# Optimization experiments

Measured on AMD Instinct MI355X. Metric: run time of the kernel, lower is better.

Reference implementation:

```python
import jax, jax.numpy as jnp
import numpy as np

B, S, D = 2, 2048, 768
E, L = 4, 2
H = 4 * D  # dim_mlp = dim * mlp_ratio
EPS = 1e-6


def setup_inputs() -> dict:
    key = jax.random.key(0)
    ks = jax.random.split(key, 4)
    x = jax.random.normal(ks[0], (B, S, D), dtype=jnp.float32)
    expert_idx = jax.random.randint(ks[1], (B, S), 0, E, dtype=jnp.int32)
    # Linear weights: normal(std=0.02), biases zero (per init_weights).
    W1 = 0.02 * jax.random.normal(ks[2], (L, E, D, H), dtype=jnp.float32)
    b1 = jnp.zeros((L, E, H), dtype=jnp.float32)
    W2 = 0.02 * jax.random.normal(ks[3], (L, E, H, D), dtype=jnp.float32)
    b2 = jnp.zeros((L, E, D), dtype=jnp.float32)
    # LayerNorm: weight=1, bias=0 (per init_weights).
    ln_g = jnp.ones((L, D), dtype=jnp.float32)
    ln_b = jnp.zeros((L, D), dtype=jnp.float32)
    return {"x": x, "expert_idx": expert_idx, "W1": W1, "b1": b1,
            "W2": W2, "b2": b2, "ln_g": ln_g, "ln_b": ln_b}


def _layernorm(x, g, b):
    mu = jnp.mean(x, axis=-1, keepdims=True)
    var = jnp.mean(jnp.square(x - mu), axis=-1, keepdims=True)
    return (x - mu) * jax.lax.rsqrt(var + EPS) * g + b


def reference(x, expert_idx, W1, b1, W2, b2, ln_g, ln_b):
    # Eval mode: Dropout and DropPath are identity.
    idx = expert_idx[:, :, None, None]  # [B,S,1,1] for gather over expert axis
    for i in range(L):
        h = _layernorm(x, ln_g[i], ln_b[i])                       # [B,S,D]
        # All experts' FFNs computed densely (as in the torch module).
        a = jnp.einsum('bsd,edh->bseh', h, W1[i]) + b1[i]         # [B,S,E,H]
        a = jax.nn.gelu(a, approximate=False)                     # exact GELU (nn.GELU)
        y = jnp.einsum('bseh,ehd->bsed', a, W2[i]) + b2[i]        # [B,S,E,D] == feat_all
        # Per-token gather of the selected expert's slice.
        sel = jnp.take_along_axis(y, idx, axis=2)[:, :, 0, :]     # [B,S,D]
        x = x + sel
    return x
```

## Files before the change

### kernel.cpp

```cpp
#include <hip/hip_runtime.h>
#include <hip/hip_bf16.h>

#define T_TOK 4096
#define DD 768
#define HH 3072
#define EE 4
#define LL 2

typedef __attribute__((ext_vector_type(8))) short short8;
typedef __attribute__((ext_vector_type(4))) float f32x4;

__device__ __forceinline__ float bf2f(ushort u) { return __uint_as_float(((unsigned)u) << 16); }
__device__ __forceinline__ ushort f2bf(float f) {
  unsigned x = __float_as_uint(f);
  return (ushort)((x + 0x7fffu + ((x >> 16) & 1u)) >> 16);
}

__device__ __forceinline__ void gl2lds16(const void* g, void* l) {
  __builtin_amdgcn_global_load_lds((const __attribute__((address_space(1))) void*)g,
                                   (__attribute__((address_space(3))) void*)l, 16, 0, 0);
}

__global__ __launch_bounds__(256) void prep_kernel(const int* __restrict__ eidx,
                                                   int* __restrict__ perm,
                                                   int* __restrict__ inv,
                                                   int* __restrict__ meta) {
  __shared__ int cnt[EE], cur[EE], offs[EE];
  int t = threadIdx.x;
  if (t < EE) { cnt[t] = 0; cur[t] = 0; }
  __syncthreads();
  for (int i = t; i < T_TOK; i += 256) atomicAdd(&cnt[eidx[i]], 1);
  __syncthreads();
  if (t == 0) {
    int off = 0, nt = 0;
    for (int e = 0; e < EE; e++) {
      meta[e] = off; offs[e] = off;
      int c = cnt[e];
      int n = (c + 127) >> 7;
      for (int k = 0; k < n; k++) { meta[6 + nt] = e; meta[46 + nt] = k << 7; nt++; }
      off += c;
    }
    meta[4] = off;
    meta[5] = nt;
  }
  __syncthreads();
  for (int i = t; i < T_TOK; i += 256) {
    int e = eidx[i];
    int pos = offs[e] + atomicAdd(&cur[e], 1);
    perm[pos] = i;
    inv[i] = pos;
  }
}

__global__ __launch_bounds__(256) void cvt_kernel(const float* __restrict__ x,
                                                  float* __restrict__ xf, int n) {
  int i = blockIdx.x * 256 + threadIdx.x;
  int stride = gridDim.x * 256;
  for (; i < n; i += stride) xf[i] = x[i];
}

__global__ __launch_bounds__(256) void store_kernel(const float* __restrict__ xf,
                                                    float* __restrict__ out, int n) {
  int i = blockIdx.x * 256 + threadIdx.x;
  int stride = gridDim.x * 256;
  for (; i < n; i += stride) out[i] = xf[i];
}

__global__ __launch_bounds__(256) void ln_kernel(const float* __restrict__ xf,
                                                 const float* __restrict__ g,
                                                 const float* __restrict__ b,
                                                 const int* __restrict__ inv,
                                                 ushort* __restrict__ h) {
  int wid = blockIdx.x * 4 + (threadIdx.x >> 6);
  int lane = threadIdx.x & 63;
  const float* xr = xf + (size_t)wid * DD;
  float v[12], s = 0.f, ss = 0.f;
#pragma unroll
  for (int i = 0; i < 12; i++) {
    v[i] = xr[lane + i * 64];
    s += v[i]; ss += v[i] * v[i];
  }
#pragma unroll
  for (int o = 32; o; o >>= 1) { s += __shfl_xor(s, o, 64); ss += __shfl_xor(ss, o, 64); }
  float mu = s * (1.f / DD);
  float var = ss * (1.f / DD) - mu * mu;
  float rs = rsqrtf(var + 1e-6f);
  ushort* hr = h + (size_t)inv[wid] * DD;
#pragma unroll
  for (int i = 0; i < 12; i++) {
    int c = lane + i * 64;
    hr[c] = f2bf((v[i] - mu) * rs * g[c] + b[c]);
  }
}

__global__ __launch_bounds__(256) void transpose_f32_bf16(const float* __restrict__ src,
                                                          ushort* __restrict__ dst,
                                                          int R, int C) {
  __shared__ ushort tile[64][68];
  size_t mo = (size_t)blockIdx.z * R * C;
  src += mo;
  dst += mo;
  int c0 = blockIdx.x * 64, r0 = blockIdx.y * 64;
  int t = threadIdx.x;
  int tr = t >> 4;
  int tc = (t & 15) << 2;
#pragma unroll
  for (int i = 0; i < 4; i++) {
    int r = tr + i * 16;
    float4 v = *(const float4*)(src + (size_t)(r0 + r) * C + (c0 + tc));
    tile[r][tc] = f2bf(v.x); tile[r][tc + 1] = f2bf(v.y);
    tile[r][tc + 2] = f2bf(v.z); tile[r][tc + 3] = f2bf(v.w);
  }
  __syncthreads();
#pragma unroll
  for (int i = 0; i < 4; i++) {
    int c = tr + i * 16;
    ushort4 v;
    v.x = tile[tc][c]; v.y = tile[tc + 1][c]; v.z = tile[tc + 2][c]; v.w = tile[tc + 3][c];
    *(ushort4*)(dst + (size_t)(c0 + c) * R + (r0 + tc)) = v;
  }
}

template <int KTOT, int KLEN, int NTOT, bool GELU>
__global__ __launch_bounds__(256) void gemm_kernel(const ushort* __restrict__ A,
                                                   const ushort* __restrict__ Bt,
                                                   const float* __restrict__ bias,
                                                   void* __restrict__ Cout,
                                                   const int* __restrict__ perm,
                                                   const int* __restrict__ meta) {
  int ty = blockIdx.y;
  if (ty >= meta[5]) return;
  int e = meta[6 + ty];
  int mstart = meta[46 + ty];
  int off0 = meta[e];
  int cnt = meta[e + 1] - off0;
  if (cnt <= 0) return;
  int ntile = blockIdx.x;
  int kbegin = blockIdx.z * KLEN;

  __shared__ __align__(16) ushort lds[16384];
  ushort* As = lds;
  ushort* Bs = lds + 8192;

  int tid = threadIdx.x;
  int w = tid >> 6, lane = tid & 63;

  int rr = lane >> 3;
  int koff = (lane & 7) * 8;
  const ushort* agp[4];
  const ushort* bgp[4];
  ushort* alp[4];
  ushort* blp[4];
#pragma unroll
  for (int i = 0; i < 4; i++) {
    int r = w * 32 + i * 8 + rr;
    int arow = off0 + min(mstart + r, cnt - 1);
    int brow = e * NTOT + ntile * 128 + r;
    agp[i] = A + (size_t)arow * KTOT + kbegin + koff;
    bgp[i] = Bt + (size_t)brow * KTOT + kbegin + koff;
    alp[i] = As + r * 64 + koff;
    blp[i] = Bs + r * 64 + koff;
  }

  int wm = (w >> 1) * 64, wn = (w & 1) * 64;
  int qm = lane & 15;
  int qk = (lane >> 4) * 8;

  f32x4 acc[4][4];
#pragma unroll
  for (int mi = 0; mi < 4; mi++)
#pragma unroll
    for (int ni = 0; ni < 4; ni++) acc[mi][ni] = (f32x4){0.f, 0.f, 0.f, 0.f};

  for (int k0 = 0; k0 < KLEN; k0 += 64) {
#pragma unroll
    for (int i = 0; i < 4; i++) {
      gl2lds16(agp[i] + k0, alp[i]);
      gl2lds16(bgp[i] + k0, blp[i]);
    }
    __syncthreads();
#pragma unroll
    for (int h2 = 0; h2 < 2; h2++) {
      short8 af[4], bfr[4];
#pragma unroll
      for (int mi = 0; mi < 4; mi++)
        af[mi] = *(const short8*)(As + (wm + mi * 16 + qm) * 64 + h2 * 32 + qk);
#pragma unroll
      for (int ni = 0; ni < 4; ni++)
        bfr[ni] = *(const short8*)(Bs + (wn + ni * 16 + qm) * 64 + h2 * 32 + qk);
#pragma unroll
      for (int mi = 0; mi < 4; mi++)
#pragma unroll
        for (int ni = 0; ni < 4; ni++)
          acc[mi][ni] = __builtin_amdgcn_mfma_f32_16x16x32_bf16(af[mi], bfr[ni], acc[mi][ni], 0, 0, 0);
    }
    __syncthreads();
  }

  int rbase = (lane >> 4) * 4;
  if (GELU) {
    float bv[4];
#pragma unroll
    for (int ni = 0; ni < 4; ni++)
      bv[ni] = bias[e * NTOT + ntile * 128 + wn + ni * 16 + qm];
#pragma unroll
    for (int mi = 0; mi < 4; mi++)
#pragma unroll
      for (int ni = 0; ni < 4; ni++) {
        int c = wn + ni * 16 + qm;
#pragma unroll
        for (int r = 0; r < 4; r++) {
          float vv = acc[mi][ni][r] + bv[ni];
          vv = 0.5f * vv * (1.f + erff(vv * 0.70710678118f));
          lds[(wm + mi * 16 + rbase + r) * 128 + c] = f2bf(vv);
        }
      }
    __syncthreads();
    int row0 = tid >> 4;
    int cseg = (tid & 15) * 8;
    ushort* aout = (ushort*)Cout;
#pragma unroll
    for (int it = 0; it < 8; it++) {
      int row = it * 16 + row0;
      int mg = mstart + row;
      if (mg < cnt) {
        short8 v = *(const short8*)(lds + row * 128 + cseg);
        *(short8*)(aout + (size_t)(off0 + mg) * HH + ntile * 128 + cseg) = v;
      }
    }
  } else {
    float* xf = (float*)Cout;
    float bv[4];
#pragma unroll
    for (int ni = 0; ni < 4; ni++)
      bv[ni] = (blockIdx.z == 0) ? bias[e * NTOT + ntile * 128 + wn + ni * 16 + qm] : 0.f;
#pragma unroll
    for (int mi = 0; mi < 4; mi++) {
#pragma unroll
      for (int r = 0; r < 4; r++) {
        int mg = mstart + wm + mi * 16 + rbase + r;
        if (mg >= cnt) continue;
        int token = perm[off0 + mg];
        float* crow = xf + (size_t)token * DD + ntile * 128;
#pragma unroll
        for (int ni = 0; ni < 4; ni++)
          atomicAdd(&crow[wn + ni * 16 + qm], acc[mi][ni][r] + bv[ni]);
      }
    }
  }
}

extern "C" void kernel_launch(void* const* d_in, const int* in_sizes, int n_in,
                              void* d_out, int out_size, void* d_ws, size_t ws_size,
                              hipStream_t stream) {
  const float* x   = (const float*)d_in[0];
  const int*   eidx = (const int*)d_in[1];
  const float* W1  = (const float*)d_in[2];
  const float* b1  = (const float*)d_in[3];
  const float* W2  = (const float*)d_in[4];
  const float* b2  = (const float*)d_in[5];
  const float* lng = (const float*)d_in[6];
  const float* lnb = (const float*)d_in[7];

  char* ws = (char*)d_ws;
  float*  xf   = (float*)(ws + 0);
  ushort* h    = (ushort*)(ws + 12582912);
  ushort* a    = (ushort*)(ws + 18874368);
  ushort* Wt   = (ushort*)(ws + 44040192);
  int*    perm = (int*)(ws + 62914560);
  int*    inv  = (int*)(ws + 62930944);
  int*    meta = (int*)(ws + 62947328);

  const int NELT = T_TOK * DD;

  prep_kernel<<<1, 256, 0, stream>>>(eidx, perm, inv, meta);
  cvt_kernel<<<3072, 256, 0, stream>>>(x, xf, NELT);

  for (int l = 0; l < LL; l++) {
    ln_kernel<<<T_TOK / 4, 256, 0, stream>>>(xf, lng + l * DD, lnb + l * DD, inv, h);
    transpose_f32_bf16<<<dim3(HH / 64, DD / 64, EE), 256, 0, stream>>>(
        W1 + (size_t)l * EE * DD * HH, Wt, DD, HH);
    gemm_kernel<DD, DD, HH, true><<<dim3(HH / 128, 36), 256, 0, stream>>>(
        h, Wt, b1 + l * EE * HH, (void*)a, perm, meta);
    transpose_f32_bf16<<<dim3(DD / 64, HH / 64, EE), 256, 0, stream>>>(
        W2 + (size_t)l * EE * HH * DD, Wt, HH, DD);
    gemm_kernel<HH, HH / 2, DD, false><<<dim3(DD / 128, 36, 2), 256, 0, stream>>>(
        a, Wt, b2 + l * EE * DD, (void*)xf, perm, meta);
  }

  store_kernel<<<3072, 256, 0, stream>>>(xf, (float*)d_out, NELT);
}
```

Measured before the change: 440.6 us.

## Replace atomic scatter with split-K partial buffers, smaller M tiles, swizzled LDS

The down-projection GEMM now writes its two split-K partials as plain stores into sorted-order buffers instead of atomically adding into the token-order residual. The residual sum is folded into the next layer's LayerNorm and into a final store kernel, and the copy-in kernel and perm array are removed. GEMM M tiles shrink from 128 to 64 rows with an XOR-swizzled LDS layout, which gives more blocks and fewer bank conflicts. The cost is extra partial-buffer traffic and lower per-block reuse of the B tiles.

```diff
diff --git a/kernel.cpp b/kernel.cpp
--- a/kernel.cpp
+++ b/kernel.cpp
@@ -6,6 +6,7 @@
 #define HH 3072
 #define EE 4
 #define LL 2
+#define NELT (T_TOK * DD)
 
 typedef __attribute__((ext_vector_type(8))) short short8;
 typedef __attribute__((ext_vector_type(4))) float f32x4;
@@ -22,7 +23,6 @@
 }
 
 __global__ __launch_bounds__(256) void prep_kernel(const int* __restrict__ eidx,
-                                                   int* __restrict__ perm,
                                                    int* __restrict__ inv,
                                                    int* __restrict__ meta) {
   __shared__ int cnt[EE], cur[EE], offs[EE];
@@ -36,8 +36,8 @@
     for (int e = 0; e < EE; e++) {
       meta[e] = off; offs[e] = off;
       int c = cnt[e];
-      int n = (c + 127) >> 7;
-      for (int k = 0; k < n; k++) { meta[6 + nt] = e; meta[46 + nt] = k << 7; nt++; }
+      int n = (c + 63) >> 6;
+      for (int k = 0; k < n; k++) { meta[8 + nt] = e; meta[96 + nt] = k << 6; nt++; }
       off += c;
     }
     meta[4] = off;
@@ -46,50 +46,62 @@
   __syncthreads();
   for (int i = t; i < T_TOK; i += 256) {
     int e = eidx[i];
-    int pos = offs[e] + atomicAdd(&cur[e], 1);
-    perm[pos] = i;
-    inv[i] = pos;
-  }
-}
-
-__global__ __launch_bounds__(256) void cvt_kernel(const float* __restrict__ x,
-                                                  float* __restrict__ xf, int n) {
-  int i = blockIdx.x * 256 + threadIdx.x;
-  int stride = gridDim.x * 256;
-  for (; i < n; i += stride) xf[i] = x[i];
-}
-
-__global__ __launch_bounds__(256) void store_kernel(const float* __restrict__ xf,
-                                                    float* __restrict__ out, int n) {
-  int i = blockIdx.x * 256 + threadIdx.x;
-  int stride = gridDim.x * 256;
-  for (; i < n; i += stride) out[i] = xf[i];
-}
-
-__global__ __launch_bounds__(256) void ln_kernel(const float* __restrict__ xf,
+    inv[i] = offs[e] + atomicAdd(&cur[e], 1);
+  }
+}
+
+template <bool HASY, bool WRITEX>
+__global__ __launch_bounds__(256) void ln_kernel(const float* __restrict__ x,
+                                                 const float* __restrict__ y,
                                                  const float* __restrict__ g,
                                                  const float* __restrict__ b,
                                                  const int* __restrict__ inv,
-                                                 ushort* __restrict__ h) {
+                                                 ushort* __restrict__ h,
+                                                 float* __restrict__ xf) {
   int wid = blockIdx.x * 4 + (threadIdx.x >> 6);
   int lane = threadIdx.x & 63;
-  const float* xr = xf + (size_t)wid * DD;
+  int pos = inv[wid];
+  const float* xr = x + (size_t)wid * DD;
+  const float* y0 = y + (size_t)pos * DD;
+  const float* y1 = y0 + NELT;
   float v[12], s = 0.f, ss = 0.f;
 #pragma unroll
   for (int i = 0; i < 12; i++) {
-    v[i] = xr[lane + i * 64];
-    s += v[i]; ss += v[i] * v[i];
+    int c = lane + i * 64;
+    float vv = xr[c];
+    if (HASY) vv += y0[c] + y1[c];
+    if (WRITEX) xf[(size_t)wid * DD + c] = vv;
+    v[i] = vv;
+    s += vv; ss += vv * vv;
   }
 #pragma unroll
   for (int o = 32; o; o >>= 1) { s += __shfl_xor(s, o, 64); ss += __shfl_xor(ss, o, 64); }
   float mu = s * (1.f / DD);
   float var = ss * (1.f / DD) - mu * mu;
   float rs = rsqrtf(var + 1e-6f);
-  ushort* hr = h + (size_t)inv[wid] * DD;
+  ushort* hr = h + (size_t)pos * DD;
 #pragma unroll
   for (int i = 0; i < 12; i++) {
     int c = lane + i * 64;
     hr[c] = f2bf((v[i] - mu) * rs * g[c] + b[c]);
+  }
+}
+
+__global__ __launch_bounds__(256) void store_kernel(const float* __restrict__ xf,
+                                                    const float* __restrict__ y,
+                                                    const int* __restrict__ inv,
+                                                    float* __restrict__ out) {
+  int wid = blockIdx.x * 4 + (threadIdx.x >> 6);
+  int lane = threadIdx.x & 63;
+  int pos = inv[wid];
+  const float* xr = xf + (size_t)wid * DD;
+  const float* y0 = y + (size_t)pos * DD;
+  const float* y1 = y0 + NELT;
+  float* o = out + (size_t)wid * DD;
+#pragma unroll
+  for (int i = 0; i < 12; i++) {
+    int c = lane + i * 64;
+    o[c] = xr[c] + y0[c] + y1[c];
   }
 }
 
@@ -122,74 +134,78 @@
 }
 
 template <int KTOT, int KLEN, int NTOT, bool GELU>
-__global__ __launch_bounds__(256) void gemm_kernel(const ushort* __restrict__ A,
-                                                   const ushort* __restrict__ Bt,
-                                                   const float* __restrict__ bias,
-                                                   void* __restrict__ Cout,
-                                                   const int* __restrict__ perm,
-                                                   const int* __restrict__ meta) {
+__global__ __launch_bounds__(256, 4) void gemm_kernel(const ushort* __restrict__ A,
+                                                      const ushort* __restrict__ Bt,
+                                                      const float* __restrict__ bias,
+                                                      void* __restrict__ Cout,
+                                                      const int* __restrict__ meta) {
   int ty = blockIdx.y;
   if (ty >= meta[5]) return;
-  int e = meta[6 + ty];
-  int mstart = meta[46 + ty];
+  int e = meta[8 + ty];
+  int mstart = meta[96 + ty];
   int off0 = meta[e];
   int cnt = meta[e + 1] - off0;
-  if (cnt <= 0) return;
   int ntile = blockIdx.x;
-  int kbegin = blockIdx.z * KLEN;
-
-  __shared__ __align__(16) ushort lds[16384];
+  int z = blockIdx.z;
+  int kbegin = z * KLEN;
+
+  __shared__ __align__(16) ushort lds[12288];
   ushort* As = lds;
-  ushort* Bs = lds + 8192;
+  ushort* Bs = lds + 4096;
 
   int tid = threadIdx.x;
   int w = tid >> 6, lane = tid & 63;
 
   int rr = lane >> 3;
-  int koff = (lane & 7) * 8;
-  const ushort* agp[4];
+  int swz = ((lane & 7) ^ rr) * 8;
+  const ushort* agp[2];
   const ushort* bgp[4];
-  ushort* alp[4];
+  ushort* alp[2];
   ushort* blp[4];
 #pragma unroll
+  for (int i = 0; i < 2; i++) {
+    int r = w * 16 + i * 8;
+    int arow = off0 + min(mstart + r + rr, cnt - 1);
+    agp[i] = A + (size_t)arow * KTOT + kbegin + swz;
+    alp[i] = As + r * 64 + lane * 8;
+  }
+#pragma unroll
   for (int i = 0; i < 4; i++) {
-    int r = w * 32 + i * 8 + rr;
-    int arow = off0 + min(mstart + r, cnt - 1);
-    int brow = e * NTOT + ntile * 128 + r;
-    agp[i] = A + (size_t)arow * KTOT + kbegin + koff;
-    bgp[i] = Bt + (size_t)brow * KTOT + kbegin + koff;
-    alp[i] = As + r * 64 + koff;
-    blp[i] = Bs + r * 64 + koff;
-  }
-
-  int wm = (w >> 1) * 64, wn = (w & 1) * 64;
+    int r = w * 32 + i * 8;
+    int brow = e * NTOT + ntile * 128 + r + rr;
+    bgp[i] = Bt + (size_t)brow * KTOT + kbegin + swz;
+    blp[i] = Bs + r * 64 + lane * 8;
+  }
+
+  int wm = (w >> 1) * 32, wn = (w & 1) * 64;
   int qm = lane & 15;
-  int qk = (lane >> 4) * 8;
-
-  f32x4 acc[4][4];
-#pragma unroll
-  for (int mi = 0; mi < 4; mi++)
+  int quad = lane >> 4;
+  int s7 = qm & 7;
+
+  f32x4 acc[2][4];
+#pragma unroll
+  for (int mi = 0; mi < 2; mi++)
 #pragma unroll
     for (int ni = 0; ni < 4; ni++) acc[mi][ni] = (f32x4){0.f, 0.f, 0.f, 0.f};
 
   for (int k0 = 0; k0 < KLEN; k0 += 64) {
 #pragma unroll
-    for (int i = 0; i < 4; i++) {
-      gl2lds16(agp[i] + k0, alp[i]);
-      gl2lds16(bgp[i] + k0, blp[i]);
-    }
+    for (int i = 0; i < 2; i++) gl2lds16(agp[i] + k0, alp[i]);
+#pragma unroll
+    for (int i = 0; i < 4; i++) gl2lds16(bgp[i] + k0, blp[i]);
     __syncthreads();
 #pragma unroll
     for (int h2 = 0; h2 < 2; h2++) {
-      short8 af[4], bfr[4];
-#pragma unroll
-      for (int mi = 0; mi < 4; mi++)
-        af[mi] = *(const short8*)(As + (wm + mi * 16 + qm) * 64 + h2 * 32 + qk);
+      int lchunk = ((h2 * 4 + quad) ^ s7) * 8;
+      short8 af[2], bfr[4];
+#pragma unroll
+      for (int mi = 0; mi < 2; mi++)
+        af[mi] = *(const short8*)(As + (wm + mi * 16 + qm) * 64 + lchunk);
 #pragma unroll
       for (int ni = 0; ni < 4; ni++)
-        bfr[ni] = *(const short8*)(Bs + (wn + ni * 16 + qm) * 64 + h2 * 32 + qk);
-#pragma unroll
-      for (int mi = 0; mi < 4; mi++)
+        bfr[ni] = *(const short8*)(Bs + (wn + ni * 16 + qm) * 64 + lchunk);
+#pragma unroll
+      for (int mi = 0; mi < 2; mi++)
 #pragma unroll
         for (int ni = 0; ni < 4; ni++)
           acc[mi][ni] = __builtin_amdgcn_mfma_f32_16x16x32_bf16(af[mi], bfr[ni], acc[mi][ni], 0, 0, 0);
@@ -197,14 +213,15 @@
     __syncthreads();
   }
 
-  int rbase = (lane >> 4) * 4;
+  int rbase = quad * 4;
+  float bv[4];
+#pragma unroll
+  for (int ni = 0; ni < 4; ni++)
+    bv[ni] = (!GELU && z != 0) ? 0.f : bias[e * NTOT + ntile * 128 + wn + ni * 16 + qm];
+
   if (GELU) {
-    float bv[4];
-#pragma unroll
-    for (int ni = 0; ni < 4; ni++)
-      bv[ni] = bias[e * NTOT + ntile * 128 + wn + ni * 16 + qm];
-#pragma unroll
-    for (int mi = 0; mi < 4; mi++)
+#pragma unroll
+    for (int mi = 0; mi < 2; mi++)
 #pragma unroll
       for (int ni = 0; ni < 4; ni++) {
         int c = wn + ni * 16 + qm;
@@ -220,7 +237,7 @@
     int cseg = (tid & 15) * 8;
     ushort* aout = (ushort*)Cout;
 #pragma unroll
-    for (int it = 0; it < 8; it++) {
+    for (int it = 0; it < 4; it++) {
       int row = it * 16 + row0;
       int mg = mstart + row;
       if (mg < cnt) {
@@ -229,22 +246,17 @@
       }
     }
   } else {
-    float* xf = (float*)Cout;
-    float bv[4];
-#pragma unroll
-    for (int ni = 0; ni < 4; ni++)
-      bv[ni] = (blockIdx.z == 0) ? bias[e * NTOT + ntile * 128 + wn + ni * 16 + qm] : 0.f;
-#pragma unroll
-    for (int mi = 0; mi < 4; mi++) {
+    float* y = (float*)Cout + (size_t)z * NELT;
+#pragma unroll
+    for (int mi = 0; mi < 2; mi++) {
 #pragma unroll
       for (int r = 0; r < 4; r++) {
         int mg = mstart + wm + mi * 16 + rbase + r;
         if (mg >= cnt) continue;
-        int token = perm[off0 + mg];
-        float* crow = xf + (size_t)token * DD + ntile * 128;
+        float* crow = y + (size_t)(off0 + mg) * DD + ntile * 128;
 #pragma unroll
         for (int ni = 0; ni < 4; ni++)
-          atomicAdd(&crow[wn + ni * 16 + qm], acc[mi][ni][r] + bv[ni]);
+          crow[wn + ni * 16 + qm] = acc[mi][ni][r] + bv[ni];
       }
     }
   }
@@ -254,7 +266,7 @@
                               void* d_out, int out_size, void* d_ws, size_t ws_size,
                               hipStream_t stream) {
   const float* x   = (const float*)d_in[0];
-  const int*   eidx = (const int*)d_in[1];
+  const int*  eidx = (const int*)d_in[1];
   const float* W1  = (const float*)d_in[2];
   const float* b1  = (const float*)d_in[3];
   const float* W2  = (const float*)d_in[4];
@@ -267,26 +279,28 @@
   ushort* h    = (ushort*)(ws + 12582912);
   ushort* a    = (ushort*)(ws + 18874368);
   ushort* Wt   = (ushort*)(ws + 44040192);
-  int*    perm = (int*)(ws + 62914560);
-  int*    inv  = (int*)(ws + 62930944);
-  int*    meta = (int*)(ws + 62947328);
-
-  const int NELT = T_TOK * DD;
-
-  prep_kernel<<<1, 256, 0, stream>>>(eidx, perm, inv, meta);
-  cvt_kernel<<<3072, 256, 0, stream>>>(x, xf, NELT);
+  float*  y    = (float*)(ws + 62914560);
+  int*    inv  = (int*)(ws + 88080384);
+  int*    meta = (int*)(ws + 88096768);
+
+  prep_kernel<<<1, 256, 0, stream>>>(eidx, inv, meta);
 
   for (int l = 0; l < LL; l++) {
-    ln_kernel<<<T_TOK / 4, 256, 0, stream>>>(xf, lng + l * DD, lnb + l * DD, inv, h);
+    if (l == 0)
+      ln_kernel<false, false><<<T_TOK / 4, 256, 0, stream>>>(
+          x, y, lng, lnb, inv, h, xf);
+    else
+      ln_kernel<true, true><<<T_TOK / 4, 256, 0, stream>>>(
+          x, y, lng + l * DD, lnb + l * DD, inv, h, xf);
     transpose_f32_bf16<<<dim3(HH / 64, DD / 64, EE), 256, 0, stream>>>(
         W1 + (size_t)l * EE * DD * HH, Wt, DD, HH);
-    gemm_kernel<DD, DD, HH, true><<<dim3(HH / 128, 36), 256, 0, stream>>>(
-        h, Wt, b1 + l * EE * HH, (void*)a, perm, meta);
+    gemm_kernel<DD, DD, HH, true><<<dim3(HH / 128, 68), 256, 0, stream>>>(
+        h, Wt, b1 + l * EE * HH, (void*)a, meta);
     transpose_f32_bf16<<<dim3(DD / 64, HH / 64, EE), 256, 0, stream>>>(
         W2 + (size_t)l * EE * HH * DD, Wt, HH, DD);
-    gemm_kernel<HH, HH / 2, DD, false><<<dim3(DD / 128, 36, 2), 256, 0, stream>>>(
-        a, Wt, b2 + l * EE * DD, (void*)xf, perm, meta);
-  }
-
-  store_kernel<<<3072, 256, 0, stream>>>(xf, (float*)d_out, NELT);
-}
+    gemm_kernel<HH, HH / 2, DD, false><<<dim3(DD / 128, 68, 2), 256, 0, stream>>>(
+        a, Wt, b2 + l * EE * DD, (void*)y, meta);
+  }
+
+  store_kernel<<<T_TOK / 4, 256, 0, stream>>>(xf, y, inv, (float*)d_out);
+}
```

New measurement: 392.4 us. 10.9% less time.
